# Kernel optimization log

Measured on AMD Instinct MI355X. Metric: run time of the kernel, lower is better.

The kernel has to match this reference:

```python
import jax, jax.numpy as jnp
import numpy as np

N = 100000      # nodes
DEG = 16        # fixed degree
E = N * DEG     # edges
C_IN = 128
C_OUT = 128


def setup_inputs() -> dict:
    key = jax.random.key(0)
    k1, k2, k3, k4, k5 = jax.random.split(key, 5)
    x = jax.random.normal(k1, (N, C_IN), dtype=jnp.float32)
    # glorot-ish init for the dense weight
    scale = jnp.sqrt(6.0 / (C_IN + C_OUT)).astype(jnp.float32)
    weight = jax.random.uniform(k2, (C_IN, C_OUT), dtype=jnp.float32, minval=-1.0, maxval=1.0) * scale
    bias = jax.random.normal(k3, (C_OUT,), dtype=jnp.float32) * 0.02
    # fixed-degree CSR: every node has DEG in-edges; CSC analogously
    rowptr = (jnp.arange(N + 1, dtype=jnp.int32) * DEG)
    colind = jax.random.randint(k4, (E,), 0, N, dtype=jnp.int32)
    colptr = (jnp.arange(N + 1, dtype=jnp.int32) * DEG)
    rowind = jax.random.randint(k5, (E,), 0, N, dtype=jnp.int32)
    return {"x": x, "weight": weight, "bias": bias,
            "rowptr": rowptr, "colind": colind,
            "colptr": colptr, "rowind": rowind}


def _deg_inv_sqrt(indptr, dtype):
    deg = (indptr[1:] - indptr[:-1]).astype(dtype)
    return (1.0 / jnp.sqrt(deg))[:, None]  # [N, 1]


def reference(x, weight, bias, rowptr, colind, colptr, rowind):
    # dense transform: [N, C_in] @ [C_in, C_out]
    h = x @ weight
    in_norm = _deg_inv_sqrt(rowptr, h.dtype)    # 1/sqrt(in-degree)
    out_norm = _deg_inv_sqrt(colptr, h.dtype)   # 1/sqrt(out-degree)
    h = h * out_norm
    # CSR SpMM (unweighted): out[i] = sum_{e in [rowptr[i], rowptr[i+1])} h[colind[e]]
    n_nodes = rowptr.shape[0] - 1
    n_edges = colind.shape[0]
    row = jnp.searchsorted(rowptr, jnp.arange(n_edges, dtype=rowptr.dtype), side="right") - 1
    aggr = jax.ops.segment_sum(h[colind], row, num_segments=n_nodes)
    aggr = aggr * in_norm + bias
    return aggr
```

## Files before the change

kernel.cpp:

```cpp
#include <hip/hip_runtime.h>
#include <hip/hip_bf16.h>

#define N_NODES 100000
#define DEG 16
#define C 128
#define NTILES 6250
#define FBLOCKS 1024

typedef __attribute__((ext_vector_type(8))) short short8;
typedef __attribute__((ext_vector_type(4))) float f32x4;

__device__ inline unsigned short f2bf(float f) {
    unsigned int u = __builtin_bit_cast(unsigned int, f);
    u += 0x7fffu + ((u >> 16) & 1u);
    return (unsigned short)(u >> 16);
}

__global__ __launch_bounds__(256, 8)
void gcn_prep_kernel(const float* __restrict__ x, const int* __restrict__ colptr,
                     unsigned char* __restrict__ x8, float* __restrict__ scale)
{
    int tid = threadIdx.x;
    int wave = tid >> 6;
    int lane = tid & 63;
    int row = (blockIdx.x * 4 + wave) * 4 + (lane >> 4);
    int cg = lane & 15;

    const float* xr = x + (long)row * C + cg * 8;
    f32x4 a = *reinterpret_cast<const f32x4*>(xr);
    f32x4 b = *reinterpret_cast<const f32x4*>(xr + 4);

    float m = fmaxf(fmaxf(fmaxf(fabsf(a[0]), fabsf(a[1])), fmaxf(fabsf(a[2]), fabsf(a[3]))),
                    fmaxf(fmaxf(fabsf(b[0]), fabsf(b[1])), fmaxf(fabsf(b[2]), fabsf(b[3]))));
    m = fmaxf(m, __shfl_xor(m, 1));
    m = fmaxf(m, __shfl_xor(m, 2));
    m = fmaxf(m, __shfl_xor(m, 4));
    m = fmaxf(m, __shfl_xor(m, 8));
    m = fmaxf(m, 1e-30f);

    float inv = 127.0f / m;
    unsigned int lo = 0, hi = 0;
    lo |= ((unsigned int)((int)rintf(a[0] * inv) + 128));
    lo |= ((unsigned int)((int)rintf(a[1] * inv) + 128)) << 8;
    lo |= ((unsigned int)((int)rintf(a[2] * inv) + 128)) << 16;
    lo |= ((unsigned int)((int)rintf(a[3] * inv) + 128)) << 24;
    hi |= ((unsigned int)((int)rintf(b[0] * inv) + 128));
    hi |= ((unsigned int)((int)rintf(b[1] * inv) + 128)) << 8;
    hi |= ((unsigned int)((int)rintf(b[2] * inv) + 128)) << 16;
    hi |= ((unsigned int)((int)rintf(b[3] * inv) + 128)) << 24;

    uint2 pk; pk.x = lo; pk.y = hi;
    *reinterpret_cast<uint2*>(x8 + (long)row * C + cg * 8) = pk;

    if (cg == 0) {
        int od = colptr[row + 1] - colptr[row];
        scale[row] = m * (1.0f / 127.0f) * rsqrtf((float)od);
    }
}

__device__ __forceinline__ uint4 dq_pack(const uint2* v, float mysc, int gb, float innorm)
{
    float acc[8] = {0.f, 0.f, 0.f, 0.f, 0.f, 0.f, 0.f, 0.f};
    float ssum = 0.f;
#pragma unroll
    for (int e = 0; e < 16; ++e) {
        float s = __shfl(mysc, gb + e);
        ssum += s;
        unsigned int a = v[e].x, b = v[e].y;
        acc[0] += s * (float)(a & 0xff);
        acc[1] += s * (float)((a >> 8) & 0xff);
        acc[2] += s * (float)((a >> 16) & 0xff);
        acc[3] += s * (float)(a >> 24);
        acc[4] += s * (float)(b & 0xff);
        acc[5] += s * (float)((b >> 8) & 0xff);
        acc[6] += s * (float)((b >> 16) & 0xff);
        acc[7] += s * (float)(b >> 24);
    }
    float fix = 128.0f * ssum;
    uint4 o;
    o.x = (unsigned int)f2bf((acc[0] - fix) * innorm) |
          ((unsigned int)f2bf((acc[1] - fix) * innorm) << 16);
    o.y = (unsigned int)f2bf((acc[2] - fix) * innorm) |
          ((unsigned int)f2bf((acc[3] - fix) * innorm) << 16);
    o.z = (unsigned int)f2bf((acc[4] - fix) * innorm) |
          ((unsigned int)f2bf((acc[5] - fix) * innorm) << 16);
    o.w = (unsigned int)f2bf((acc[6] - fix) * innorm) |
          ((unsigned int)f2bf((acc[7] - fix) * innorm) << 16);
    return o;
}

__global__ __launch_bounds__(256, 4)
void gcn_fused_kernel(const unsigned char* __restrict__ x8,
                      const float* __restrict__ scale,
                      const int* __restrict__ rowptr,
                      const int* __restrict__ colind,
                      const float* __restrict__ wmat,
                      const float* __restrict__ bias,
                      float* __restrict__ out)
{
    __shared__ uint4 atile[2][16 * 16];

    int tid  = threadIdx.x;
    int wv   = tid >> 6;
    int lane = tid & 63;
    int g    = lane >> 4;
    int cl   = lane & 15;
    int gb   = lane & 48;

    short8 bw[2][4];
    float  bv[2];
#pragma unroll
    for (int n = 0; n < 2; ++n) {
        int nt = wv * 2 + n;
#pragma unroll
        for (int kc = 0; kc < 4; ++kc) {
            short8 b;
#pragma unroll
            for (int j = 0; j < 8; ++j)
                b[j] = (short)f2bf(wmat[(kc * 32 + g * 8 + j) * C + nt * 16 + cl]);
            bw[n][kc] = b;
        }
        bv[n] = bias[nt * 16 + cl];
    }

    int t = blockIdx.x;

    {
        int node = t * 16 + wv * 4 + g;
        int base = rowptr[node];
        float innorm = rsqrtf((float)(rowptr[node + 1] - base));
        int myidx = colind[base + cl];
        float mysc = scale[myidx];
        uint2 v[16];
#pragma unroll
        for (int e = 0; e < 16; ++e) {
            int j = __shfl(myidx, gb + e);
            v[e] = *reinterpret_cast<const uint2*>(x8 + (j << 7) + (cl << 3));
        }
        int r = wv * 4 + g;
        atile[0][r * 16 + (cl ^ (r & 7))] = dq_pack(v, mysc, gb, innorm);
    }
    __syncthreads();

    int p = 0;
    while (true) {
        int nxt = t + FBLOCKS;
        bool more = nxt < NTILES;

        int nidx = 0; float nsc = 0.f, ninn = 0.f;
        uint2 nv[16];
        if (more) {
            int nn = nxt * 16 + wv * 4 + g;
            int nb = rowptr[nn];
            ninn = rsqrtf((float)(rowptr[nn + 1] - nb));
            nidx = colind[nb + cl];
            nsc = scale[nidx];
#pragma unroll
            for (int e = 0; e < 16; ++e) {
                int j = __shfl(nidx, gb + e);
                nv[e] = *reinterpret_cast<const uint2*>(x8 + (j << 7) + (cl << 3));
            }
        }

        short8 af[4];
#pragma unroll
        for (int kc = 0; kc < 4; ++kc)
            af[kc] = __builtin_bit_cast(short8,
                atile[p][cl * 16 + ((kc * 4 + g) ^ (cl & 7))]);

#pragma unroll
        for (int n = 0; n < 2; ++n) {
            f32x4 acc = {0.f, 0.f, 0.f, 0.f};
#pragma unroll
            for (int kc = 0; kc < 4; ++kc)
                acc = __builtin_amdgcn_mfma_f32_16x16x32_bf16(af[kc], bw[n][kc], acc, 0, 0, 0);
            float* op = out + (long)(t * 16 + g * 4) * C + (wv * 2 + n) * 16 + cl;
#pragma unroll
            for (int r2 = 0; r2 < 4; ++r2)
                op[r2 * C] = acc[r2] + bv[n];
        }

        if (!more) break;

        {
            int r = wv * 4 + g;
            atile[p ^ 1][r * 16 + (cl ^ (r & 7))] = dq_pack(nv, nsc, gb, ninn);
        }
        __syncthreads();
        t = nxt;
        p ^= 1;
    }
}

extern "C" void kernel_launch(void* const* d_in, const int* in_sizes, int n_in,
                              void* d_out, int out_size, void* d_ws, size_t ws_size,
                              hipStream_t stream) {
    const float* x      = (const float*)d_in[0];
    const float* w      = (const float*)d_in[1];
    const float* bias   = (const float*)d_in[2];
    const int*   rowptr = (const int*)d_in[3];
    const int*   colind = (const int*)d_in[4];
    const int*   colptr = (const int*)d_in[5];
    float* out = (float*)d_out;

    unsigned char* x8    = (unsigned char*)d_ws;
    float*         scale = (float*)((char*)d_ws + (size_t)N_NODES * C);

    gcn_prep_kernel<<<6250, 256, 0, stream>>>(x, colptr, x8, scale);
    gcn_fused_kernel<<<FBLOCKS, 256, 0, stream>>>(x8, scale, rowptr, colind,
                                                  w, bias, out);
}
```

Baseline: 155.8 us.

## Give each wave its own 16-node tile with LDS-resident weight fragments

The fused kernel now keeps the full bf16 weight matrix in LDS in MFMA fragment order. Each wave processes an independent 16-node tile and computes all 8 output column tiles, so the per-tile block-wide __syncthreads and the cross-iteration double-buffered prefetch go away. Gathers are issued two nodes at a time to raise memory-level parallelism. The grid and launch bounds are reduced to fit the larger LDS and register footprint, which may lower occupancy and remove the explicit software prefetch overlap.

```diff
diff --git a/kernel.cpp b/kernel.cpp
--- a/kernel.cpp
+++ b/kernel.cpp
@@ -5,7 +5,7 @@
 #define DEG 16
 #define C 128
 #define NTILES 6250
-#define FBLOCKS 1024
+#define FBLOCKS 782
 
 typedef __attribute__((ext_vector_type(8))) short short8;
 typedef __attribute__((ext_vector_type(4))) float f32x4;
@@ -89,7 +89,7 @@
     return o;
 }
 
-__global__ __launch_bounds__(256, 4)
+__global__ __launch_bounds__(256, 3)
 void gcn_fused_kernel(const unsigned char* __restrict__ x8,
                       const float* __restrict__ scale,
                       const int* __restrict__ rowptr,
@@ -98,7 +98,8 @@
                       const float* __restrict__ bias,
                       float* __restrict__ out)
 {
-    __shared__ uint4 atile[2][16 * 16];
+    __shared__ unsigned short wfrag[32 * 64 * 8];
+    __shared__ uint4 atile[4][16 * 16];
 
     int tid  = threadIdx.x;
     int wv   = tid >> 6;
@@ -107,88 +108,78 @@
     int cl   = lane & 15;
     int gb   = lane & 48;
 
-    short8 bw[2][4];
-    float  bv[2];
-#pragma unroll
-    for (int n = 0; n < 2; ++n) {
-        int nt = wv * 2 + n;
-#pragma unroll
-        for (int kc = 0; kc < 4; ++kc) {
-            short8 b;
-#pragma unroll
-            for (int j = 0; j < 8; ++j)
-                b[j] = (short)f2bf(wmat[(kc * 32 + g * 8 + j) * C + nt * 16 + cl]);
-            bw[n][kc] = b;
+    for (int i0 = tid * 4; i0 < C * C; i0 += 1024) {
+        f32x4 ww = *reinterpret_cast<const f32x4*>(wmat + i0);
+#pragma unroll
+        for (int d = 0; d < 4; ++d) {
+            int i = i0 + d;
+            int k = i >> 7, n = i & 127;
+            int nt = n >> 4, lr = n & 15;
+            int kc = k >> 5, quad = (k >> 3) & 3, j = k & 7;
+            wfrag[((((nt << 2) + kc) << 6) + (quad << 4) + lr) * 8 + j] = f2bf(ww[d]);
         }
-        bv[n] = bias[nt * 16 + cl];
-    }
-
-    int t = blockIdx.x;
-
-    {
-        int node = t * 16 + wv * 4 + g;
-        int base = rowptr[node];
-        float innorm = rsqrtf((float)(rowptr[node + 1] - base));
-        int myidx = colind[base + cl];
-        float mysc = scale[myidx];
-        uint2 v[16];
-#pragma unroll
-        for (int e = 0; e < 16; ++e) {
-            int j = __shfl(myidx, gb + e);
-            v[e] = *reinterpret_cast<const uint2*>(x8 + (j << 7) + (cl << 3));
+    }
+    __syncthreads();
+
+    float bv[8];
+#pragma unroll
+    for (int nt = 0; nt < 8; ++nt) bv[nt] = bias[nt * 16 + cl];
+
+    uint4* myat = atile[wv];
+
+    for (int t = blockIdx.x * 4 + wv; t < NTILES; t += FBLOCKS * 4) {
+#pragma unroll
+        for (int pr = 0; pr < 2; ++pr) {
+            int r0 = pr * 2, r1 = pr * 2 + 1;
+            int node0 = t * 16 + g * 4 + r0;
+            int node1 = t * 16 + g * 4 + r1;
+            int b0 = rowptr[node0];
+            int b1 = rowptr[node1];
+            float in0 = rsqrtf((float)(rowptr[node0 + 1] - b0));
+            float in1 = rsqrtf((float)(rowptr[node1 + 1] - b1));
+            int i0 = colind[b0 + cl];
+            int i1 = colind[b1 + cl];
+            float s0 = scale[i0];
+            float s1 = scale[i1];
+
+            uint2 v0[16], v1[16];
+#pragma unroll
+            for (int e = 0; e < 16; ++e) {
+                int j = __shfl(i0, gb + e);
+                v0[e] = *reinterpret_cast<const uint2*>(x8 + (j << 7) + (cl << 3));
+            }
+#pragma unroll
+            for (int e = 0; e < 16; ++e) {
+                int j = __shfl(i1, gb + e);
+                v1[e] = *reinterpret_cast<const uint2*>(x8 + (j << 7) + (cl << 3));
+            }
+            int rr0 = g * 4 + r0, rr1 = g * 4 + r1;
+            myat[rr0 * 16 + (cl ^ (rr0 & 7))] = dq_pack(v0, s0, gb, in0);
+            myat[rr1 * 16 + (cl ^ (rr1 & 7))] = dq_pack(v1, s1, gb, in1);
         }
-        int r = wv * 4 + g;
-        atile[0][r * 16 + (cl ^ (r & 7))] = dq_pack(v, mysc, gb, innorm);
-    }
-    __syncthreads();
-
-    int p = 0;
-    while (true) {
-        int nxt = t + FBLOCKS;
-        bool more = nxt < NTILES;
-
-        int nidx = 0; float nsc = 0.f, ninn = 0.f;
-        uint2 nv[16];
-        if (more) {
-            int nn = nxt * 16 + wv * 4 + g;
-            int nb = rowptr[nn];
-            ninn = rsqrtf((float)(rowptr[nn + 1] - nb));
-            nidx = colind[nb + cl];
-            nsc = scale[nidx];
-#pragma unroll
-            for (int e = 0; e < 16; ++e) {
-                int j = __shfl(nidx, gb + e);
-                nv[e] = *reinterpret_cast<const uint2*>(x8 + (j << 7) + (cl << 3));
-            }
-        }
+
+        asm volatile("s_waitcnt lgkmcnt(0)" ::: "memory");
 
         short8 af[4];
 #pragma unroll
         for (int kc = 0; kc < 4; ++kc)
             af[kc] = __builtin_bit_cast(short8,
-                atile[p][cl * 16 + ((kc * 4 + g) ^ (cl & 7))]);
-
-#pragma unroll
-        for (int n = 0; n < 2; ++n) {
+                myat[cl * 16 + ((kc * 4 + g) ^ (cl & 7))]);
+
+#pragma unroll
+        for (int nt = 0; nt < 8; ++nt) {
             f32x4 acc = {0.f, 0.f, 0.f, 0.f};
 #pragma unroll
-            for (int kc = 0; kc < 4; ++kc)
-                acc = __builtin_amdgcn_mfma_f32_16x16x32_bf16(af[kc], bw[n][kc], acc, 0, 0, 0);
-            float* op = out + (long)(t * 16 + g * 4) * C + (wv * 2 + n) * 16 + cl;
-#pragma unroll
-            for (int r2 = 0; r2 < 4; ++r2)
-                op[r2 * C] = acc[r2] + bv[n];
+            for (int kc = 0; kc < 4; ++kc) {
+                short8 b = *reinterpret_cast<const short8*>(
+                    &wfrag[((((nt << 2) + kc) << 6) + lane) * 8]);
+                acc = __builtin_amdgcn_mfma_f32_16x16x32_bf16(af[kc], b, acc, 0, 0, 0);
+            }
+            float* op = out + (long)(t * 16 + g * 4) * C + nt * 16 + cl;
+#pragma unroll
+            for (int r = 0; r < 4; ++r)
+                op[r * C] = acc[r] + bv[nt];
         }
-
-        if (!more) break;
-
-        {
-            int r = wv * 4 + g;
-            atile[p ^ 1][r * 16 + (cl ^ (r & 7))] = dq_pack(nv, nsc, gb, ninn);
-        }
-        __syncthreads();
-        t = nxt;
-        p ^= 1;
     }
 }
 
```

Result: slower. 166.9 us (+7.1%).
